# Kernel tuning notes

Hardware: AMD Instinct MI355X
Metric: run time of the kernel (lower is better)

The kernel has to match this reference:

```python
import jax, jax.numpy as jnp
import numpy as np

# Winograd F(2x2, 3x3) transform matrices (standard Lavin & Gray form).
# The original torch module encodes B^T / A^T but applies them with elementwise
# mul (a bug that crashes); the intended math is Y = A^T [ (G g G^T) .* (B^T d B) ] A
# per 4x4 input tile with stride 2, which equals a valid 3x3 conv. We implement
# that intended Winograd computation faithfully and vectorized.
_BT = jnp.array([[1., 0., -1., 0.],
                 [0., 1., 1., 0.],
                 [0., -1., 1., 0.],
                 [0., 1., 0., -1.]], dtype=jnp.float32)
_G = jnp.array([[1., 0., 0.],
                [0.5, 0.5, 0.5],
                [0.5, -0.5, 0.5],
                [0., 0., 1.]], dtype=jnp.float32)
_AT = jnp.array([[1., 1., 1., 0.],
                 [0., 1., -1., -1.]], dtype=jnp.float32)


def setup_inputs() -> dict:
    key = jax.random.key(0)
    k1, k2 = jax.random.split(key)
    X = jax.random.normal(k1, (16, 32, 258, 258), dtype=jnp.float32)
    K = jax.random.normal(k2, (32, 32, 3, 3), dtype=jnp.float32)
    return {"X": X, "K": K}


def _winograd_conv(X, K):
    B_, C, H, W = X.shape
    Fo = K.shape[0]
    blocks = (H - 3) // 2 + 1  # number of 2x2 output tiles per spatial dim

    # Kernel transform: U = G K G^T  -> (Fo, C, 4, 4)
    U = jnp.einsum('ij,fcjk,lk->fcil', _G, K, _G)

    # Extract overlapping 4x4 tiles with stride 2: (B, C, blocks, blocks, 4, 4)
    i0 = jnp.arange(blocks) * 2
    win = i0[:, None] + jnp.arange(4)[None, :]          # (blocks, 4)
    tiles = X[:, :, win, :]                              # (B, C, blocks, 4, W)
    tiles = tiles[:, :, :, :, win]                       # (B, C, blocks, 4, blocks, 4)
    tiles = tiles.transpose(0, 1, 2, 4, 3, 5)            # (B, C, p, q, 4, 4)

    # Input transform: V = B^T d B
    V = jnp.einsum('ij,bcpqjk,lk->bcpqil', _BT, tiles, _BT)

    # Elementwise multiply in transform domain, summed over input channels
    M = jnp.einsum('fcil,bcpqil->bfpqil', U, V)          # (B, Fo, p, q, 4, 4)

    # Inverse transform: Y = A^T M A -> (B, Fo, p, q, 2, 2)
    Y = jnp.einsum('ij,bfpqjk,lk->bfpqil', _AT, M, _AT)

    # Stitch 2x2 tiles back: (B, Fo, 2*blocks, 2*blocks)
    out = Y.transpose(0, 1, 2, 4, 3, 5).reshape(B_, Fo, 2 * blocks, 2 * blocks)
    return out


def reference(X, K):
    return _winograd_conv(X, K)
```

## Files before the change

kernel.cpp:

```cpp
#include <hip/hip_runtime.h>
#include <stdint.h>

typedef __attribute__((ext_vector_type(8))) short bf16x8;
typedef __attribute__((ext_vector_type(4))) float f32x4;

__device__ inline float bflo(uint32_t w) { union { uint32_t i; float f; } v; v.i = w << 16; return v.f; }
__device__ inline float bfhi(uint32_t w) { union { uint32_t i; float f; } v; v.i = w & 0xffff0000u; return v.f; }
__device__ inline uint32_t f2bf(float f) { union { float f; uint32_t i; } v; v.f = f; return (v.i + 0x8000u) >> 16; }
__device__ inline uint32_t pk(float lo, float hi) { return f2bf(lo) | (f2bf(hi) << 16); }

__global__ __launch_bounds__(256) void wg_filter(const float* __restrict__ Kk, uint32_t* __restrict__ Ud)
{
    const int idx = blockIdx.x * 256 + threadIdx.x;
    if (idx >= 512) return;
    const int cp = idx & 15, f = idx >> 4;
    float u[2][16];
    #pragma unroll
    for (int h = 0; h < 2; h++) {
        const float* kp = Kk + (f * 32 + cp * 2 + h) * 9;
        float k00 = kp[0], k01 = kp[1], k02 = kp[2];
        float k10 = kp[3], k11 = kp[4], k12 = kp[5];
        float k20 = kp[6], k21 = kp[7], k22 = kp[8];
        float t[4][3];
        t[0][0] = k00; t[0][1] = k01; t[0][2] = k02;
        t[1][0] = 0.5f * (k00 + k10 + k20); t[1][1] = 0.5f * (k01 + k11 + k21); t[1][2] = 0.5f * (k02 + k12 + k22);
        t[2][0] = 0.5f * (k00 - k10 + k20); t[2][1] = 0.5f * (k01 - k11 + k21); t[2][2] = 0.5f * (k02 - k12 + k22);
        t[3][0] = k20; t[3][1] = k21; t[3][2] = k22;
        #pragma unroll
        for (int i = 0; i < 4; i++) {
            float a0 = t[i][0], a1 = t[i][1], a2 = t[i][2];
            u[h][i * 4 + 0] = a0;
            u[h][i * 4 + 1] = 0.5f * (a0 + a1 + a2);
            u[h][i * 4 + 2] = 0.5f * (a0 - a1 + a2);
            u[h][i * 4 + 3] = a2;
        }
    }
    const int base = ((cp >> 2) * 32 + f) * 4 + (cp & 3);
    #pragma unroll
    for (int p = 0; p < 16; p++) Ud[p * 512 + base] = pk(u[0][p], u[1][p]);
}

__global__ __launch_bounds__(256, 3) void wg_main(
    const float* __restrict__ X, const uint16_t* __restrict__ U, float* __restrict__ out)
{
    __shared__ __align__(16) uint32_t Pl[2896];
    __shared__ __align__(16) uint16_t Vl[16384];

    const int tid = threadIdx.x;
    const int qb = blockIdx.x;
    const int pb = blockIdx.y;
    const int b  = blockIdx.z;
    const int y0 = pb * 8, x0 = qb * 16;

    for (int s = tid; s < 1440; s += 256) {
        const int pr = s / 90;
        const int r  = s - pr * 90;
        const int row = r / 9, seg = r - row * 9;
        const float* g0 = X + ((size_t)((b * 32 + pr * 2) * 258 + y0 + row)) * 258 + x0 + seg * 2;
        float2 a = *(const float2*)g0;
        float2 c = *(const float2*)(g0 + 258 * 258);
        const int pbase = pr * 181 + row * 18 + seg * 2;
        Pl[pbase]     = pk(a.x, c.x);
        Pl[pbase + 1] = pk(a.y, c.y);
    }
    __syncthreads();

    uint32_t* vp = (uint32_t*)Vl;
    #pragma unroll
    for (int it = 0; it < 2; it++) {
        const int rem  = it * 4 + (tid >> 6);
        const int tblk = rem & 1, cpH = rem >> 1;
        const int cp2  = tid & 3, t15 = (tid >> 2) & 15;
        const int cp   = cpH * 4 + cp2;
        const int tt   = tblk * 16 + t15;
        const int tr   = tt >> 3, tc = tt & 7;
        const uint32_t* pp = &Pl[cp * 181 + (tr * 2) * 18 + tc * 2];
        float d0[4][4], d1[4][4];
        #pragma unroll
        for (int j = 0; j < 4; j++)
            #pragma unroll
            for (int k = 0; k < 4; k++) {
                uint32_t w = pp[j * 18 + k];
                d0[j][k] = bflo(w); d1[j][k] = bfhi(w);
            }
        float b0[4][4], b1[4][4];
        #pragma unroll
        for (int k = 0; k < 4; k++) {
            b0[0][k] = d0[0][k] - d0[2][k];  b1[0][k] = d1[0][k] - d1[2][k];
            b0[1][k] = d0[1][k] + d0[2][k];  b1[1][k] = d1[1][k] + d1[2][k];
            b0[2][k] = d0[2][k] - d0[1][k];  b1[2][k] = d1[2][k] - d1[1][k];
            b0[3][k] = d0[1][k] - d0[3][k];  b1[3][k] = d1[1][k] - d1[3][k];
        }
        const int vbase = ((tblk * 4 + cpH) * 16 + t15) * 4 + cp2;
        #pragma unroll
        for (int i = 0; i < 4; i++) {
            float v00 = b0[i][0] - b0[i][2], v10 = b1[i][0] - b1[i][2];
            float v01 = b0[i][1] + b0[i][2], v11 = b1[i][1] + b1[i][2];
            float v02 = b0[i][2] - b0[i][1], v12 = b1[i][2] - b1[i][1];
            float v03 = b0[i][1] - b0[i][3], v13 = b1[i][1] - b1[i][3];
            vp[(i * 4 + 0) * 512 + vbase] = pk(v00, v10);
            vp[(i * 4 + 1) * 512 + vbase] = pk(v01, v11);
            vp[(i * 4 + 2) * 512 + vbase] = pk(v02, v12);
            vp[(i * 4 + 3) * 512 + vbase] = pk(v03, v13);
        }
    }
    __syncthreads();

    const int wave = tid >> 6, lane = tid & 63;
    const int fh = wave & 1, tb = wave >> 1;
    const int l15 = lane & 15, lq = lane >> 4;
    const uint16_t* Ub = U + (lq * 32 + fh * 16 + l15) * 8;
    const uint16_t* Vb = Vl + ((tb * 4 + lq) * 16 + l15) * 8;

    float y[4][4];
    #pragma unroll
    for (int r = 0; r < 4; r++)
        #pragma unroll
        for (int j = 0; j < 4; j++) y[r][j] = 0.f;

    #pragma unroll
    for (int ch = 0; ch < 2; ch++) {
        f32x4 acc[8];
        #pragma unroll
        for (int p8 = 0; p8 < 8; p8++) acc[p8] = (f32x4){0.f, 0.f, 0.f, 0.f};
        #pragma unroll
        for (int p8 = 0; p8 < 8; p8++) {
            const int p = ch * 8 + p8;
            bf16x8 a = *(const bf16x8*)(Ub + p * 1024);
            bf16x8 v = *(const bf16x8*)(Vb + p * 1024);
            acc[p8] = __builtin_amdgcn_mfma_f32_16x16x32_bf16(a, v, acc[p8], 0, 0, 0);
        }
        #pragma unroll
        for (int r = 0; r < 4; r++) {
            #pragma unroll
            for (int ii = 0; ii < 2; ii++) {
                const int i = ch * 2 + ii;
                float m0 = acc[ii * 4 + 0][r], m1 = acc[ii * 4 + 1][r];
                float m2 = acc[ii * 4 + 2][r], m3 = acc[ii * 4 + 3][r];
                float c0 = m0 + m1 + m2, c1 = m1 - m2 - m3;
                if (i == 0)      { y[r][0] += c0; y[r][1] += c1; }
                else if (i == 1) { y[r][0] += c0; y[r][1] += c1; y[r][2] += c0; y[r][3] += c1; }
                else if (i == 2) { y[r][0] += c0; y[r][1] += c1; y[r][2] -= c0; y[r][3] -= c1; }
                else             { y[r][2] -= c0; y[r][3] -= c1; }
            }
        }
    }

    const int t = tb * 16 + l15;
    const int trr = t >> 3, tcc = t & 7;
    const int p = pb * 4 + trr, q = qb * 8 + tcc;
    #pragma unroll
    for (int r = 0; r < 4; r++) {
        const int f = fh * 16 + lq * 4 + r;
        float* op = out + ((size_t)(b * 32 + f) * 256 + 2 * p) * 256 + 2 * q;
        *(float2*)op = make_float2(y[r][0], y[r][1]);
        *(float2*)(op + 256) = make_float2(y[r][2], y[r][3]);
    }
}

__device__ inline uint16_t f2bf16_rne(float f) {
    union { float f; uint32_t i; } v; v.f = f;
    uint32_t x = v.i;
    uint32_t r = x + 0x7fffu + ((x >> 16) & 1u);
    return (uint16_t)(r >> 16);
}
__global__ __launch_bounds__(256) void winograd_fallback(
    const float* __restrict__ X, const float* __restrict__ K, float* __restrict__ out)
{
    __shared__ uint16_t Ul[16384];
    __shared__ uint16_t Vl[16384];
    __shared__ uint16_t Pl[32 * 242];
    const int tid = threadIdx.x;
    const int qb = blockIdx.x, pb = blockIdx.y, b = blockIdx.z;
    for (int idx = tid; idx < 1024; idx += 256) {
        const int f = idx >> 5, c = idx & 31;
        const float* kp = K + (f * 32 + c) * 9;
        float k00 = kp[0], k01 = kp[1], k02 = kp[2];
        float k10 = kp[3], k11 = kp[4], k12 = kp[5];
        float k20 = kp[6], k21 = kp[7], k22 = kp[8];
        float t[4][3];
        t[0][0] = k00; t[0][1] = k01; t[0][2] = k02;
        t[1][0] = 0.5f * (k00 + k10 + k20); t[1][1] = 0.5f * (k01 + k11 + k21); t[1][2] = 0.5f * (k02 + k12 + k22);
        t[2][0] = 0.5f * (k00 - k10 + k20); t[2][1] = 0.5f * (k01 - k11 + k21); t[2][2] = 0.5f * (k02 - k12 + k22);
        t[3][0] = k20; t[3][1] = k21; t[3][2] = k22;
        const int ubase = ((c >> 3) * 32 + f) * 8 + (c & 7);
        #pragma unroll
        for (int i = 0; i < 4; i++) {
            float a0 = t[i][0], a1 = t[i][1], a2 = t[i][2];
            Ul[(i * 4 + 0) * 1024 + ubase] = f2bf16_rne(a0);
            Ul[(i * 4 + 1) * 1024 + ubase] = f2bf16_rne(0.5f * (a0 + a1 + a2));
            Ul[(i * 4 + 2) * 1024 + ubase] = f2bf16_rne(0.5f * (a0 - a1 + a2));
            Ul[(i * 4 + 3) * 1024 + ubase] = f2bf16_rne(a2);
        }
    }
    const int y0 = pb * 8, x0 = qb * 16;
    for (int s = tid; s < 2880; s += 256) {
        const int c = s / 90;
        const int r = s % 90;
        const int row = r / 9, seg = r % 9;
        const float* gp = X + ((b * 32 + c) * 258 + (y0 + row)) * 258 + x0 + seg * 2;
        float2 g = *(const float2*)gp;
        uint32_t packed = (uint32_t)f2bf16_rne(g.x) | ((uint32_t)f2bf16_rne(g.y) << 16);
        *(uint32_t*)&Pl[c * 242 + row * 24 + seg * 2] = packed;
    }
    __syncthreads();
    for (int idx = tid; idx < 1024; idx += 256) {
        const int c = idx & 31, tt = idx >> 5;
        const int tr = tt >> 3, tc = tt & 7;
        const uint16_t* pp = &Pl[c * 242 + (tr * 2) * 24 + tc * 2];
        float d[4][4];
        #pragma unroll
        for (int j = 0; j < 4; j++) {
            uint32_t w0 = *(const uint32_t*)&pp[j * 24];
            uint32_t w1 = *(const uint32_t*)&pp[j * 24 + 2];
            d[j][0] = bflo(w0 << 16 >> 16 << 16), d[j][0] = bflo(w0); d[j][1] = bfhi(w0);
            d[j][2] = bflo(w1); d[j][3] = bfhi(w1);
        }
        float bt[4][4];
        #pragma unroll
        for (int k = 0; k < 4; k++) {
            bt[0][k] = d[0][k] - d[2][k];
            bt[1][k] = d[1][k] + d[2][k];
            bt[2][k] = d[2][k] - d[1][k];
            bt[3][k] = d[1][k] - d[3][k];
        }
        const int vbase = (((tt >> 4) * 4 + (c >> 3)) * 16 + (tt & 15)) * 8 + (c & 7);
        #pragma unroll
        for (int i = 0; i < 4; i++) {
            float b0 = bt[i][0], b1 = bt[i][1], b2 = bt[i][2], b3 = bt[i][3];
            Vl[(i * 4 + 0) * 1024 + vbase] = f2bf16_rne(b0 - b2);
            Vl[(i * 4 + 1) * 1024 + vbase] = f2bf16_rne(b1 + b2);
            Vl[(i * 4 + 2) * 1024 + vbase] = f2bf16_rne(b2 - b1);
            Vl[(i * 4 + 3) * 1024 + vbase] = f2bf16_rne(b1 - b3);
        }
    }
    __syncthreads();
    const int wave = tid >> 6, lane = tid & 63;
    const int fh = wave & 1, tb = wave >> 1;
    const int l15 = lane & 15, lq = lane >> 4;
    f32x4 acc[16];
    #pragma unroll
    for (int p = 0; p < 16; p++) acc[p] = (f32x4){0.f, 0.f, 0.f, 0.f};
    #pragma unroll
    for (int p = 0; p < 16; p++) {
        bf16x8 a = *(const bf16x8*)&Ul[p * 1024 + (lq * 32 + fh * 16 + l15) * 8];
        bf16x8 bv = *(const bf16x8*)&Vl[p * 1024 + ((tb * 4 + lq) * 16 + l15) * 8];
        acc[p] = __builtin_amdgcn_mfma_f32_16x16x32_bf16(a, bv, acc[p], 0, 0, 0);
    }
    #pragma unroll
    for (int r = 0; r < 4; r++) {
        const int f = fh * 16 + lq * 4 + r;
        const int t = tb * 16 + l15;
        const int tr = t >> 3, tc = t & 7;
        const int p = pb * 4 + tr, q = qb * 8 + tc;
        float m[4][4];
        #pragma unroll
        for (int i = 0; i < 4; i++)
            #pragma unroll
            for (int l = 0; l < 4; l++)
                m[i][l] = acc[i * 4 + l][r];
        float s0[4], s1[4];
        #pragma unroll
        for (int k = 0; k < 4; k++) {
            s0[k] = m[0][k] + m[1][k] + m[2][k];
            s1[k] = m[1][k] - m[2][k] - m[3][k];
        }
        float* op = out + ((size_t)(b * 32 + f) * 256 + 2 * p) * 256 + 2 * q;
        *(float2*)op = make_float2(s0[0] + s0[1] + s0[2], s0[1] - s0[2] - s0[3]);
        *(float2*)(op + 256) = make_float2(s1[0] + s1[1] + s1[2], s1[1] - s1[2] - s1[3]);
    }
}

extern "C" void kernel_launch(void* const* d_in, const int* in_sizes, int n_in,
                              void* d_out, int out_size, void* d_ws, size_t ws_size,
                              hipStream_t stream) {
    const float* X = (const float*)d_in[0];
    const float* K = (const float*)d_in[1];
    float* out = (float*)d_out;
    dim3 grid(16, 32, 16);
    if (ws_size >= 32768) {
        wg_filter<<<2, 256, 0, stream>>>(K, (uint32_t*)d_ws);
        wg_main<<<grid, 256, 0, stream>>>(X, (const uint16_t*)d_ws, out);
    } else {
        winograd_fallback<<<grid, 256, 0, stream>>>(X, K, out);
    }
}
```

Measured before the change: 95.75 us.

## Split input transform into two half-passes to halve LDS and raise occupancy

The Winograd input transform is now computed in two halves, two transform rows per pass, interleaved with the MFMA chunks that consume them. This lets the V buffer in shared memory shrink by half, and the launch bound is raised from 3 to 5 blocks per CU to use the freed LDS for occupancy. In exchange it adds an extra barrier between passes and recomputes some column partial sums, which could cost latency or raise register pressure under the tighter launch bound. A redundant duplicate assignment in a secondary kernel is also removed.

Measured after the change: 95.42 us. Within noise of the previous version (-0.3%).

```diff
diff --git a/kernel.cpp b/kernel.cpp
--- a/kernel.cpp
+++ b/kernel.cpp
@@ -40,11 +40,11 @@
     for (int p = 0; p < 16; p++) Ud[p * 512 + base] = pk(u[0][p], u[1][p]);
 }
 
-__global__ __launch_bounds__(256, 3) void wg_main(
+__global__ __launch_bounds__(256, 5) void wg_main(
     const float* __restrict__ X, const uint16_t* __restrict__ U, float* __restrict__ out)
 {
     __shared__ __align__(16) uint32_t Pl[2896];
-    __shared__ __align__(16) uint16_t Vl[16384];
+    __shared__ __align__(16) uint16_t Vl[8192];
 
     const int tid = threadIdx.x;
     const int qb = blockIdx.x;
@@ -65,52 +65,12 @@
     }
     __syncthreads();
 
-    uint32_t* vp = (uint32_t*)Vl;
-    #pragma unroll
-    for (int it = 0; it < 2; it++) {
-        const int rem  = it * 4 + (tid >> 6);
-        const int tblk = rem & 1, cpH = rem >> 1;
-        const int cp2  = tid & 3, t15 = (tid >> 2) & 15;
-        const int cp   = cpH * 4 + cp2;
-        const int tt   = tblk * 16 + t15;
-        const int tr   = tt >> 3, tc = tt & 7;
-        const uint32_t* pp = &Pl[cp * 181 + (tr * 2) * 18 + tc * 2];
-        float d0[4][4], d1[4][4];
-        #pragma unroll
-        for (int j = 0; j < 4; j++)
-            #pragma unroll
-            for (int k = 0; k < 4; k++) {
-                uint32_t w = pp[j * 18 + k];
-                d0[j][k] = bflo(w); d1[j][k] = bfhi(w);
-            }
-        float b0[4][4], b1[4][4];
-        #pragma unroll
-        for (int k = 0; k < 4; k++) {
-            b0[0][k] = d0[0][k] - d0[2][k];  b1[0][k] = d1[0][k] - d1[2][k];
-            b0[1][k] = d0[1][k] + d0[2][k];  b1[1][k] = d1[1][k] + d1[2][k];
-            b0[2][k] = d0[2][k] - d0[1][k];  b1[2][k] = d1[2][k] - d1[1][k];
-            b0[3][k] = d0[1][k] - d0[3][k];  b1[3][k] = d1[1][k] - d1[3][k];
-        }
-        const int vbase = ((tblk * 4 + cpH) * 16 + t15) * 4 + cp2;
-        #pragma unroll
-        for (int i = 0; i < 4; i++) {
-            float v00 = b0[i][0] - b0[i][2], v10 = b1[i][0] - b1[i][2];
-            float v01 = b0[i][1] + b0[i][2], v11 = b1[i][1] + b1[i][2];
-            float v02 = b0[i][2] - b0[i][1], v12 = b1[i][2] - b1[i][1];
-            float v03 = b0[i][1] - b0[i][3], v13 = b1[i][1] - b1[i][3];
-            vp[(i * 4 + 0) * 512 + vbase] = pk(v00, v10);
-            vp[(i * 4 + 1) * 512 + vbase] = pk(v01, v11);
-            vp[(i * 4 + 2) * 512 + vbase] = pk(v02, v12);
-            vp[(i * 4 + 3) * 512 + vbase] = pk(v03, v13);
-        }
-    }
-    __syncthreads();
-
     const int wave = tid >> 6, lane = tid & 63;
     const int fh = wave & 1, tb = wave >> 1;
     const int l15 = lane & 15, lq = lane >> 4;
     const uint16_t* Ub = U + (lq * 32 + fh * 16 + l15) * 8;
     const uint16_t* Vb = Vl + ((tb * 4 + lq) * 16 + l15) * 8;
+    uint32_t* vp = (uint32_t*)Vl;
 
     float y[4][4];
     #pragma unroll
@@ -120,16 +80,58 @@
 
     #pragma unroll
     for (int ch = 0; ch < 2; ch++) {
+        #pragma unroll
+        for (int it = 0; it < 2; it++) {
+            const int rem  = it * 4 + wave;
+            const int tblk = rem & 1, cpH = rem >> 1;
+            const int cp2  = tid & 3, t15 = (tid >> 2) & 15;
+            const int cp   = cpH * 4 + cp2;
+            const int tt   = tblk * 16 + t15;
+            const int tr   = tt >> 3, tc = tt & 7;
+            const uint32_t* pp = &Pl[cp * 181 + (tr * 2 + ch) * 18 + tc * 2];
+            float d0[3][4], d1[3][4];
+            #pragma unroll
+            for (int j = 0; j < 3; j++)
+                #pragma unroll
+                for (int k = 0; k < 4; k++) {
+                    uint32_t w = pp[j * 18 + k];
+                    d0[j][k] = bflo(w); d1[j][k] = bfhi(w);
+                }
+            float e00[4], e01[4], e10[4], e11[4];
+            #pragma unroll
+            for (int k = 0; k < 4; k++) {
+                if (ch == 0) {
+                    e00[k] = d0[0][k] - d0[2][k];  e10[k] = d1[0][k] - d1[2][k];
+                    e01[k] = d0[1][k] + d0[2][k];  e11[k] = d1[1][k] + d1[2][k];
+                } else {
+                    e00[k] = d0[1][k] - d0[0][k];  e10[k] = d1[1][k] - d1[0][k];
+                    e01[k] = d0[0][k] - d0[2][k];  e11[k] = d1[0][k] - d1[2][k];
+                }
+            }
+            const int vbase = ((tblk * 4 + cpH) * 16 + t15) * 4 + cp2;
+            #pragma unroll
+            for (int row = 0; row < 2; row++) {
+                const float* e0 = row ? e01 : e00;
+                const float* e1 = row ? e11 : e10;
+                vp[(row * 4 + 0) * 512 + vbase] = pk(e0[0] - e0[2], e1[0] - e1[2]);
+                vp[(row * 4 + 1) * 512 + vbase] = pk(e0[1] + e0[2], e1[1] + e1[2]);
+                vp[(row * 4 + 2) * 512 + vbase] = pk(e0[2] - e0[1], e1[2] - e1[1]);
+                vp[(row * 4 + 3) * 512 + vbase] = pk(e0[1] - e0[3], e1[1] - e1[3]);
+            }
+        }
+        __syncthreads();
+
         f32x4 acc[8];
         #pragma unroll
         for (int p8 = 0; p8 < 8; p8++) acc[p8] = (f32x4){0.f, 0.f, 0.f, 0.f};
         #pragma unroll
         for (int p8 = 0; p8 < 8; p8++) {
-            const int p = ch * 8 + p8;
-            bf16x8 a = *(const bf16x8*)(Ub + p * 1024);
-            bf16x8 v = *(const bf16x8*)(Vb + p * 1024);
+            bf16x8 a = *(const bf16x8*)(Ub + (ch * 8 + p8) * 1024);
+            bf16x8 v = *(const bf16x8*)(Vb + p8 * 1024);
             acc[p8] = __builtin_amdgcn_mfma_f32_16x16x32_bf16(a, v, acc[p8], 0, 0, 0);
         }
+        if (ch == 0) __syncthreads();
+
         #pragma unroll
         for (int r = 0; r < 4; r++) {
             #pragma unroll
@@ -213,7 +215,7 @@
         for (int j = 0; j < 4; j++) {
             uint32_t w0 = *(const uint32_t*)&pp[j * 24];
             uint32_t w1 = *(const uint32_t*)&pp[j * 24 + 2];
-            d[j][0] = bflo(w0 << 16 >> 16 << 16), d[j][0] = bflo(w0); d[j][1] = bfhi(w0);
+            d[j][0] = bflo(w0); d[j][1] = bfhi(w0);
             d[j][2] = bflo(w1); d[j][3] = bfhi(w1);
         }
         float bt[4][4];
```
